# Kernel tuning notes

Hardware: AMD Instinct MI355X
Metric: run time of the kernel (lower is better)

## Reference

```python
import jax, jax.numpy as jnp
import numpy as np

B, K = 16, 50
IN_CH, N_CLASSES, N_ANCH = 256, 80, 3
STRIDE, FSIZE, IGNORE_THRE = 8, 76, 0.7
N_CH = 5 + N_CLASSES
ANCHORS = np.array([[10,13],[16,30],[33,23],[30,61],[62,45],[59,119],[116,90],[156,198],[373,326]], np.float32)
ALL_GRID = ANCHORS / STRIDE            # all 9 anchors in grid units
ANCH_MASK = np.array([0, 1, 2])        # layer_no = 2
MASKED = ALL_GRID[ANCH_MASK]           # (3,2) anchors used by this head


def setup_inputs():
    key = jax.random.key(0)
    k1, k2, k3, k4, k5, k6 = jax.random.split(key, 6)
    xin = jax.random.normal(k1, (B, IN_CH, FSIZE, FSIZE), jnp.float32)
    cls = jax.random.randint(k2, (B, K), 0, N_CLASSES).astype(jnp.float32)
    xy = jax.random.uniform(k3, (B, K, 2), minval=0.05, maxval=0.95)
    wh = jax.random.uniform(k4, (B, K, 2), minval=0.02, maxval=0.30)
    labels = jnp.concatenate([cls[..., None], xy, wh], -1)   # (B,K,5) [cls,xc,yc,w,h]
    oc = N_ANCH * N_CH
    conv_w = jax.random.normal(k5, (oc, IN_CH), jnp.float32) * 0.01
    conv_b = jax.random.normal(k6, (oc,), jnp.float32) * 0.01
    return {"xin": xin, "labels": labels, "conv_w": conv_w, "conv_b": conv_b}


def _yolo(xin, conv_w, conv_b, labels):
    f, C = FSIZE, N_CLASSES
    # 1x1 conv == channel matmul
    raw = jnp.einsum('bchw,oc->bohw', xin, conv_w) + conv_b[None, :, None, None]
    raw = raw.reshape(B, N_ANCH, N_CH, f, f).transpose(0, 1, 3, 4, 2)  # (B,A,f,f,85)
    # sigmoid on x,y,obj,cls; w,h stay raw
    out = jnp.concatenate([jax.nn.sigmoid(raw[..., :2]), raw[..., 2:4], jax.nn.sigmoid(raw[..., 4:])], -1)

    grid = jnp.arange(f, dtype=jnp.float32)
    mw = jnp.asarray(MASKED[:, 0]); mh = jnp.asarray(MASKED[:, 1])
    px = out[..., 0] + grid[None, None, None, :]
    py = out[..., 1] + grid[None, None, :, None]
    pw = jnp.exp(out[..., 2]) * mw[None, :, None, None]
    ph = jnp.exp(out[..., 3]) * mh[None, :, None, None]
    pred = jax.lax.stop_gradient(jnp.stack([px, py, pw, ph], -1))  # detached, like torch .data

    labels = jax.lax.stop_gradient(labels)
    valid = labels.sum(-1) > 0                  # (B,K) padding rows are all-zero
    tx = labels[..., 1] * f; ty = labels[..., 2] * f
    tw = labels[..., 3] * f; th = labels[..., 4] * f
    ii = tx.astype(jnp.int32); jj = ty.astype(jnp.int32)

    # anchor matching: IoU of [0,0,w,h] truth vs [0,0,aw,ah] ref anchors (corners at origin)
    aw = jnp.asarray(ALL_GRID[:, 0]); ah = jnp.asarray(ALL_GRID[:, 1])
    inter_a = jnp.minimum(tw[..., None], aw) * jnp.minimum(th[..., None], ah)  # (B,K,9)
    iou_a = inter_a / (tw[..., None] * th[..., None] + aw * ah - inter_a)
    best_n_all = jnp.argmax(iou_a, -1)
    best_n = best_n_all % 3
    best_mask = (best_n_all == ANCH_MASK[0]) | (best_n_all == ANCH_MASK[1]) | (best_n_all == ANCH_MASK[2])

    # pred-vs-truth IoU in cxcywh form (xyxy=False)
    pa = pred.reshape(B, -1, 4)                 # (B, A*f*f, 4)
    tb = jnp.stack([tx, ty, tw, th], -1)        # (B, K, 4)
    tl = jnp.maximum(pa[:, :, None, :2] - pa[:, :, None, 2:] * 0.5, tb[:, None, :, :2] - tb[:, None, :, 2:] * 0.5)
    br = jnp.minimum(pa[:, :, None, :2] + pa[:, :, None, 2:] * 0.5, tb[:, None, :, :2] + tb[:, None, :, 2:] * 0.5)
    en = jnp.all(tl < br, -1)
    inter = jnp.prod(br - tl, -1) * en
    area_p = pa[..., 2] * pa[..., 3]; area_t = tb[..., 2] * tb[..., 3]
    iou_p = inter / (area_p[:, :, None] + area_t[:, None, :] - inter)
    iou_p = jnp.where(valid[:, None, :], iou_p, 0.0)
    ignore = (iou_p.max(-1) > IGNORE_THRE).reshape(B, N_ANCH, f, f)
    obj_mask = 1.0 - ignore.astype(jnp.float32)

    # scatter positive targets; non-selected rows routed out-of-bounds and dropped
    sel = valid & best_mask
    bb = jnp.where(sel, jnp.arange(B)[:, None], B)
    obj_mask = obj_mask.at[bb, best_n, jj, ii].set(1.0, mode='drop')
    tgt_mask = jnp.zeros((B, N_ANCH, f, f, 4 + C)).at[bb, best_n, jj, ii].set(1.0, mode='drop')
    scale = jnp.sqrt(2.0 - tw * th / (f * f))
    tgt_scale = jnp.zeros((B, N_ANCH, f, f, 2)).at[bb, best_n, jj, ii].set(
        jnp.broadcast_to(scale[..., None], (B, K, 2)), mode='drop')
    tvals = jnp.concatenate([
        (tx - ii)[..., None], (ty - jj)[..., None],
        jnp.log(tw / mw[best_n] + 1e-16)[..., None],
        jnp.log(th / mh[best_n] + 1e-16)[..., None],
        jnp.ones((B, K, 1), jnp.float32),
        jax.nn.one_hot(labels[..., 0].astype(jnp.int32), C)], -1)  # (B,K,85)
    target = jnp.zeros((B, N_ANCH, f, f, N_CH)).at[bb, best_n, jj, ii].set(tvals, mode='drop')

    oxy = out[..., :2] * tgt_mask[..., :2]
    owh = out[..., 2:4] * tgt_mask[..., 2:4] * tgt_scale
    oob = out[..., 4] * obj_mask
    ocl = out[..., 5:] * tgt_mask[..., 4:]
    txy = target[..., :2] * tgt_mask[..., :2]
    twh = target[..., 2:4] * tgt_mask[..., 2:4] * tgt_scale
    tob = target[..., 4] * obj_mask
    tcl = target[..., 5:] * tgt_mask[..., 4:]

    def bce(p, t, w=None):
        pc = jnp.clip(p, 1e-12, 1.0 - 1e-7)
        e = -(t * jnp.log(pc) + (1.0 - t) * jnp.log(1.0 - pc))
        if w is not None:
            e = e * w
        return e.sum()

    loss_xy = bce(oxy, txy, tgt_scale * tgt_scale)
    loss_wh = 0.5 * jnp.sum((owh - twh) ** 2)
    loss_obj = bce(oob, tob)
    loss_cls = bce(ocl, tcl)
    out_m = jnp.concatenate([oxy, owh, oob[..., None], ocl], -1)
    tgt_m = jnp.concatenate([txy, twh, tob[..., None], tcl], -1)
    loss_l2 = jnp.sum((out_m - tgt_m) ** 2)
    loss = loss_xy + loss_wh + loss_obj + loss_cls
    return loss, loss_xy, loss_wh, loss_obj, loss_cls, loss_l2, out_m


def reference(xin, labels, conv_w, conv_b):
    return _yolo(xin, conv_w, conv_b, labels)
```

## Files before the change

### kernel.cpp

```cpp
#include <hip/hip_runtime.h>
#include <hip/hip_bf16.h>

#define B_   16
#define K_   50
#define CIN  256
#define F_   76
#define A_   3
#define NCH  85
#define OC   255
#define HW   (F_*F_)
#define NBLK (B_*F_)
#define NCELL (A_*F_)
#define SLAB (F_*NCH)

#define WS_BIAS_F 32768
#define WS_LAB_F  33024
#define WS_PART_F 45824
#define WS_W15_F  55552

typedef __attribute__((ext_vector_type(8))) short short8;
typedef __attribute__((ext_vector_type(4))) float f32x4;

__device__ __constant__ float AW9[9] = {1.25f, 2.0f, 4.125f, 3.75f, 7.75f, 7.375f, 14.5f, 19.5f, 46.625f};
__device__ __constant__ float AH9[9] = {1.625f, 3.75f, 2.875f, 7.625f, 5.625f, 14.875f, 11.25f, 24.75f, 40.75f};

__device__ __forceinline__ unsigned short f2bf(float f) {
    union { float f; unsigned int u; } v; v.f = f;
    unsigned int r = v.u + 0x7fffu + ((v.u >> 16) & 1u);
    return (unsigned short)(r >> 16);
}
__device__ __forceinline__ float bf2f(unsigned short b) {
    union { unsigned int u; float f; } v; v.u = ((unsigned int)b) << 16;
    return v.f;
}
__device__ __forceinline__ float sigm(float r) { return 1.0f / (1.0f + __expf(-r)); }
__device__ __forceinline__ float bce_t(float p, float tv) {
    float pc = fminf(fmaxf(p, 1e-12f), 1.0f - 1e-7f);
    return -(tv * __logf(pc) + (1.0f - tv) * __logf(1.0f - pc));
}

__global__ void prep_kernel(const float* __restrict__ conv_w, const float* __restrict__ conv_b,
                            const float* __restrict__ labels, float* __restrict__ ws) {
    int bid = blockIdx.x, t = threadIdx.x;
    if (bid < 256) {
        float v = (t < OC) ? conv_w[t * CIN + bid] : 0.0f;
        ((unsigned short*)ws)[bid * 256 + t] = f2bf(v);
    } else if (bid == 256) {
        ws[WS_BIAS_F + t] = (t < OC) ? conv_b[t] : 0.0f;
    } else if (bid == 257) {
        for (int idx = t; idx < B_ * K_; idx += 256) {
            const float* L = labels + idx * 5;
            float cls = L[0], xc = L[1], yc = L[2], wl = L[3], hl = L[4];
            float ssum = cls + xc + yc + wl + hl;
            float validf = (ssum > 0.0f) ? 1.0f : 0.0f;
            float tx = xc * F_, ty = yc * F_, tw = wl * F_, th = hl * F_;
            int ii = (int)tx, jj = (int)ty;
            float tarea = tw * th;
            float best = -1.0f; int bn = 0;
            #pragma unroll
            for (int n = 0; n < 9; n++) {
                float inter = fminf(tw, AW9[n]) * fminf(th, AH9[n]);
                float iou = inter / (tarea + AW9[n] * AH9[n] - inter);
                if (iou > best) { best = iou; bn = n; }
            }
            int a = bn % 3;
            bool self = (validf != 0.0f) && (bn < 3);
            float* R = ws + WS_LAB_F + idx * 16;
            R[0] = tx; R[1] = ty; R[2] = tw; R[3] = th;
            R[4] = validf; R[5] = self ? (float)a : -1.0f; R[6] = (float)ii; R[7] = (float)jj;
            R[8] = tx - (float)ii; R[9] = ty - (float)jj;
            R[10] = __logf(tw / AW9[a] + 1e-16f);
            R[11] = __logf(th / AH9[a] + 1e-16f);
            R[12] = sqrtf(2.0f - tarea / (float)HW);
            R[13] = cls; R[14] = 0.0f; R[15] = 0.0f;
        }
    } else {
        unsigned short* wf = (unsigned short*)(ws + WS_W15_F);
        for (int idx = t; idx < 4096; idx += 256) {
            int ks = idx >> 9, lane = (idx >> 3) & 63, jj = idx & 7;
            int row = lane & 15;
            int k = ks * 32 + (lane >> 4) * 8 + jj;
            float v = 0.0f;
            if (row < 15) v = conv_w[((row / 5) * NCH + (row % 5)) * CIN + k];
            wf[idx] = f2bf(v);
        }
    }
}

__global__ __launch_bounds__(320) void fused_kernel(const float* __restrict__ xin,
                                                    const float* __restrict__ ws,
                                                    float* __restrict__ d_out,
                                                    float* __restrict__ part) {
    __shared__ float raw5S[15 * F_];
    __shared__ float4 LAB[K_ * 4];
    __shared__ int   flagS[NCELL];
    __shared__ float omvS[NCELL];
    __shared__ float xcolS[256];
    __shared__ float redS[5][5];

    const int t = threadIdx.x;
    const int w = t >> 6, lane = t & 63;
    const int b = blockIdx.x / F_;
    const int j = blockIdx.x % F_;
    const int lr = lane & 15, q = lane >> 4;
    const int col0 = (w < 4) ? (w << 4) : 60;

    if (t < K_ * 4) LAB[t] = ((const float4*)(ws + WS_LAB_F + b * (K_ * 16)))[t];

    const unsigned short* wf15 = (const unsigned short*)(ws + WS_W15_F);
    short8 afr[8];
    #pragma unroll
    for (int ks = 0; ks < 8; ks++)
        afr[ks] = *(const short8*)&wf15[(ks * 64 + lane) * 8];

    f32x4 acc = (f32x4){0.0f, 0.0f, 0.0f, 0.0f};
    const float* xbase = xin + (size_t)b * CIN * HW + j * F_ + col0 + lr;
    #pragma unroll
    for (int ks = 0; ks < 8; ks++) {
        int kb = ks * 32 + q * 8;
        float xv[8];
        #pragma unroll
        for (int jj = 0; jj < 8; jj++) xv[jj] = xbase[(size_t)(kb + jj) * HW];
        union { short8 s; __hip_bfloat162 h[4]; } u;
        #pragma unroll
        for (int p = 0; p < 4; p++)
            u.h[p] = __float22bfloat162_rn(make_float2(xv[2 * p], xv[2 * p + 1]));
        acc = __builtin_amdgcn_mfma_f32_16x16x32_bf16(afr[ks], u.s, acc, 0, 0, 0);
    }

    const float* biasg = ws + WS_BIAS_F;
    if (w < 4 || lr >= 4) {
        #pragma unroll
        for (int r = 0; r < 4; r++) {
            int row = q * 4 + r;
            if (row < 15) {
                int o = (row / 5) * NCH + (row % 5);
                raw5S[row * F_ + col0 + lr] = acc[r] + biasg[o];
            }
        }
    }
    __syncthreads();

    float lxy = 0.0f, lwh = 0.0f, lobj = 0.0f, lcls = 0.0f, l2 = 0.0f;
    if (t < NCELL) {
        int a = t / F_, i = t - a * F_;
        float x   = sigm(raw5S[(a * 5 + 0) * F_ + i]);
        float y   = sigm(raw5S[(a * 5 + 1) * F_ + i]);
        float wr  = raw5S[(a * 5 + 2) * F_ + i];
        float hr  = raw5S[(a * 5 + 3) * F_ + i];
        float obj = sigm(raw5S[(a * 5 + 4) * F_ + i]);

        float px = x + (float)i, py = y + (float)j;
        float pw = __expf(wr) * AW9[a], ph = __expf(hr) * AH9[a];
        float hpw = pw * 0.5f, hph = ph * 0.5f;
        float areap = pw * ph;
        float fa_t = (float)a, fi_t = (float)i, fj_t = (float)j;

        float maxiou = 0.0f; int mk = -1;
        #pragma unroll 2
        for (int k = 0; k < K_; k++) {
            float4 A0 = LAB[4 * k + 0];
            float4 A1 = LAB[4 * k + 1];
            float tx = A0.x, ty = A0.y, tw = A0.z, th = A0.w;
            float tlx = fmaxf(px - hpw, tx - tw * 0.5f);
            float tly = fmaxf(py - hph, ty - th * 0.5f);
            float brx = fminf(px + hpw, tx + tw * 0.5f);
            float bry = fminf(py + hph, ty + th * 0.5f);
            float iw = brx - tlx, ih = bry - tly;
            float inter = (iw > 0.0f && ih > 0.0f) ? iw * ih : 0.0f;
            float iou = __fdividef(inter, areap + tw * th - inter);
            iou = (A1.x != 0.0f) ? iou : 0.0f;
            maxiou = fmaxf(maxiou, iou);
            bool match = (A1.y == fa_t) & (A1.z == fi_t) & (A1.w == fj_t);
            mk = match ? k : mk;
        }
        float objmask = (maxiou > 0.7f) ? 0.0f : 1.0f;

        if (mk >= 0) {
            float4 B0 = LAB[4 * mk + 2];
            float4 B1 = LAB[4 * mk + 3];
            float sc = B1.x, sc2 = sc * sc;
            float txv = B0.x, tyv = B0.y, twv = B0.z, thv = B0.w;
            lxy = (bce_t(x, txv) + bce_t(y, tyv)) * sc2;
            float dw = wr - twv, dh = hr - thv;
            lwh = 0.5f * sc2 * (dw * dw + dh * dh);
            float pco = fminf(fmaxf(obj, 1e-12f), 1.0f - 1e-7f);
            lobj = -__logf(pco);
            float dx = x - txv, dy = y - tyv, dob = obj - 1.0f;
            l2 = dx * dx + dy * dy + sc2 * (dw * dw + dh * dh) + dob * dob;
            flagS[t] = mk + 1;
            omvS[t]  = obj;
        } else {
            float oo = obj * objmask;
            if (objmask != 0.0f) {
                float pco = fminf(obj, 1.0f - 1e-7f);
                lobj = -__logf(1.0f - pco);
            }
            l2 = oo * oo;
            flagS[t] = 0;
            omvS[t]  = oo;
        }
    }
    __syncthreads();

    for (int a = 0; a < A_; a++) {
        float2* dst = (float2*)(d_out + 6 + (size_t)((b * A_ + a) * F_ + j) * SLAB);
        for (int idx2 = t; idx2 < SLAB / 2; idx2 += 320) {
            int p = idx2 << 1;
            int i0 = p / NCH, c0 = p - i0 * NCH;
            int i1 = i0, c1 = c0 + 1;
            if (c1 == NCH) { i1++; c1 = 0; }
            float v0 = (c0 == 4) ? omvS[a * F_ + i0] : 0.0f;
            float v1 = (c1 == 4) ? omvS[a * F_ + i1] : 0.0f;
            dst[idx2] = make_float2(v0, v1);
        }
    }
    __threadfence_block();
    __syncthreads();

    const unsigned short* Wtg = (const unsigned short*)ws;
    for (int k = 0; k < K_; k++) {
        float4 A1 = LAB[4 * k + 1];
        int fa = (int)A1.y;
        if (fa < 0) continue;
        if ((int)A1.w != j) continue;
        int fi = (int)A1.z;
        int cell = fa * F_ + fi;
        if (flagS[cell] != k + 1) continue;

        if (t < 256) xcolS[t] = xin[((size_t)b * CIN + t) * HW + j * F_ + fi];
        __syncthreads();
        float4 B1 = LAB[4 * k + 3];
        float sc = B1.x; int cl = (int)B1.y;
        if (t < NCH) {
            float v; int chout;
            if (t < 80) {
                int o = fa * NCH + 5 + t;
                float accv = biasg[o];
                #pragma unroll 8
                for (int kk = 0; kk < 256; kk++)
                    accv += bf2f(Wtg[kk * 256 + o]) * xcolS[kk];
                float p = sigm(accv);
                float tcv = (t == cl) ? 1.0f : 0.0f;
                lcls += bce_t(p, tcv);
                float d = p - tcv;
                l2 += d * d;
                v = p; chout = 5 + t;
            } else {
                int ch = t - 80;
                float raw = raw5S[(fa * 5 + ch) * F_ + fi];
                v = (ch == 2 || ch == 3) ? raw * sc : sigm(raw);
                chout = ch;
            }
            d_out[6 + (size_t)((b * A_ + fa) * F_ + j) * SLAB + fi * NCH + chout] = v;
        }
        __syncthreads();
    }

    #pragma unroll
    for (int off = 32; off > 0; off >>= 1) {
        lxy  += __shfl_down(lxy, off);
        lwh  += __shfl_down(lwh, off);
        lobj += __shfl_down(lobj, off);
        lcls += __shfl_down(lcls, off);
        l2   += __shfl_down(l2, off);
    }
    if (lane == 0) {
        redS[w][0] = lxy; redS[w][1] = lwh; redS[w][2] = lobj;
        redS[w][3] = lcls; redS[w][4] = l2;
    }
    __syncthreads();
    if (t == 0) {
        float* P = part + (size_t)blockIdx.x * 8;
        #pragma unroll
        for (int q2 = 0; q2 < 5; q2++)
            P[q2] = redS[0][q2] + redS[1][q2] + redS[2][q2] + redS[3][q2] + redS[4][q2];
    }
}

__global__ void finish_kernel(const float* __restrict__ part, float* __restrict__ d_out) {
    int t = threadIdx.x;
    float s0 = 0, s1 = 0, s2 = 0, s3 = 0, s4 = 0;
    for (int bidx = t; bidx < NBLK; bidx += 256) {
        const float* P = part + (size_t)bidx * 8;
        s0 += P[0]; s1 += P[1]; s2 += P[2]; s3 += P[3]; s4 += P[4];
    }
    #pragma unroll
    for (int off = 32; off > 0; off >>= 1) {
        s0 += __shfl_down(s0, off); s1 += __shfl_down(s1, off);
        s2 += __shfl_down(s2, off); s3 += __shfl_down(s3, off);
        s4 += __shfl_down(s4, off);
    }
    __shared__ float red[4][5];
    if ((t & 63) == 0) {
        int w = t >> 6;
        red[w][0] = s0; red[w][1] = s1; red[w][2] = s2; red[w][3] = s3; red[w][4] = s4;
    }
    __syncthreads();
    if (t == 0) {
        float r0 = red[0][0] + red[1][0] + red[2][0] + red[3][0];
        float r1 = red[0][1] + red[1][1] + red[2][1] + red[3][1];
        float r2 = red[0][2] + red[1][2] + red[2][2] + red[3][2];
        float r3 = red[0][3] + red[1][3] + red[2][3] + red[3][3];
        float r4 = red[0][4] + red[1][4] + red[2][4] + red[3][4];
        d_out[0] = r0 + r1 + r2 + r3;
        d_out[1] = r0; d_out[2] = r1; d_out[3] = r2; d_out[4] = r3; d_out[5] = r4;
    }
}

extern "C" void kernel_launch(void* const* d_in, const int* in_sizes, int n_in,
                              void* d_out, int out_size, void* d_ws, size_t ws_size,
                              hipStream_t stream) {
    const float* xin    = (const float*)d_in[0];
    const float* labels = (const float*)d_in[1];
    const float* conv_w = (const float*)d_in[2];
    const float* conv_b = (const float*)d_in[3];
    float* out  = (float*)d_out;
    float* ws   = (float*)d_ws;
    float* part = ws + WS_PART_F;

    prep_kernel<<<259, 256, 0, stream>>>(conv_w, conv_b, labels, ws);
    fused_kernel<<<NBLK, 320, 0, stream>>>(xin, ws, out, part);
    finish_kernel<<<1, 256, 0, stream>>>(part, out);
}
```

Baseline: 212.4 us.

## Split fused kernel into FP32 conv-loss, slab writer, and sparse target kernels

Replaces the per-row fused kernel, which ran a bf16 MFMA for 15 box channels and then wrote a slab and handled targets, with a pipeline of four kernels. The first does an FP32 CUDA-core 15-channel conv over 128-pixel tiles with two channel halves, evaluates IoU and losses for all three anchors per pixel, and appends matched targets to a list through an atomic counter. A separate writer kernel emits the mostly-zero output slabs with float4 stores, and a sparse kernel recomputes the 80 class logits for each matched cell in FP32 straight from conv_w. This removes the full bf16 weight transpose and spreads the output writes and target work across more blocks, at the cost of an extra global round trip for objectness values and more kernel launches. Results may differ slightly from before because the math is now FP32 instead of bf16.

```diff
diff --git a/kernel.cpp b/kernel.cpp
--- a/kernel.cpp
+++ b/kernel.cpp
@@ -9,30 +9,26 @@
 #define NCH  85
 #define OC   255
 #define HW   (F_*F_)
-#define NBLK (B_*F_)
-#define NCELL (A_*F_)
 #define SLAB (F_*NCH)
 
-#define WS_BIAS_F 32768
-#define WS_LAB_F  33024
-#define WS_PART_F 45824
-#define WS_W15_F  55552
-
-typedef __attribute__((ext_vector_type(8))) short short8;
-typedef __attribute__((ext_vector_type(4))) float f32x4;
+#define WS_BIAS_F 0
+#define WS_LAB_F  256
+#define WS_W15P_F 13056
+#define WS_B15_F  17152
+#define WS_CNT_F  17168
+#define WS_REC_F  17184
+#define WS_PART_F 23584
+#define WS_OMV_F  35872
+#define WS_END_F  313120
+
+#define NTL   46
+#define NCONV (B_*NTL)
+#define NREC  800
+#define NROW  (NCONV + NREC)
 
 __device__ __constant__ float AW9[9] = {1.25f, 2.0f, 4.125f, 3.75f, 7.75f, 7.375f, 14.5f, 19.5f, 46.625f};
 __device__ __constant__ float AH9[9] = {1.625f, 3.75f, 2.875f, 7.625f, 5.625f, 14.875f, 11.25f, 24.75f, 40.75f};
 
-__device__ __forceinline__ unsigned short f2bf(float f) {
-    union { float f; unsigned int u; } v; v.f = f;
-    unsigned int r = v.u + 0x7fffu + ((v.u >> 16) & 1u);
-    return (unsigned short)(r >> 16);
-}
-__device__ __forceinline__ float bf2f(unsigned short b) {
-    union { unsigned int u; float f; } v; v.u = ((unsigned int)b) << 16;
-    return v.f;
-}
 __device__ __forceinline__ float sigm(float r) { return 1.0f / (1.0f + __expf(-r)); }
 __device__ __forceinline__ float bce_t(float p, float tv) {
     float pc = fminf(fmaxf(p, 1e-12f), 1.0f - 1e-7f);
@@ -42,12 +38,9 @@
 __global__ void prep_kernel(const float* __restrict__ conv_w, const float* __restrict__ conv_b,
                             const float* __restrict__ labels, float* __restrict__ ws) {
     int bid = blockIdx.x, t = threadIdx.x;
-    if (bid < 256) {
-        float v = (t < OC) ? conv_w[t * CIN + bid] : 0.0f;
-        ((unsigned short*)ws)[bid * 256 + t] = f2bf(v);
-    } else if (bid == 256) {
+    if (bid == 0) {
         ws[WS_BIAS_F + t] = (t < OC) ? conv_b[t] : 0.0f;
-    } else if (bid == 257) {
+    } else if (bid == 1) {
         for (int idx = t; idx < B_ * K_; idx += 256) {
             const float* L = labels + idx * 5;
             float cls = L[0], xc = L[1], yc = L[2], wl = L[3], hl = L[4];
@@ -75,213 +68,235 @@
             R[13] = cls; R[14] = 0.0f; R[15] = 0.0f;
         }
     } else {
-        unsigned short* wf = (unsigned short*)(ws + WS_W15_F);
         for (int idx = t; idx < 4096; idx += 256) {
-            int ks = idx >> 9, lane = (idx >> 3) & 63, jj = idx & 7;
-            int row = lane & 15;
-            int k = ks * 32 + (lane >> 4) * 8 + jj;
+            int c = idx >> 4, r = idx & 15;
             float v = 0.0f;
-            if (row < 15) v = conv_w[((row / 5) * NCH + (row % 5)) * CIN + k];
-            wf[idx] = f2bf(v);
-        }
-    }
-}
-
-__global__ __launch_bounds__(320) void fused_kernel(const float* __restrict__ xin,
-                                                    const float* __restrict__ ws,
-                                                    float* __restrict__ d_out,
-                                                    float* __restrict__ part) {
-    __shared__ float raw5S[15 * F_];
+            if (r < 15) v = conv_w[((r / 5) * NCH + (r % 5)) * CIN + c];
+            ws[WS_W15P_F + idx] = v;
+        }
+        if (t < 16) ws[WS_B15_F + t] = (t < 15) ? conv_b[(t / 5) * NCH + (t % 5)] : 0.0f;
+        if (t == 16) *(int*)(ws + WS_CNT_F) = 0;
+    }
+}
+
+__global__ __launch_bounds__(256) void convloss_kernel(const float* __restrict__ xin,
+                                                       float* __restrict__ ws) {
     __shared__ float4 LAB[K_ * 4];
-    __shared__ int   flagS[NCELL];
-    __shared__ float omvS[NCELL];
-    __shared__ float xcolS[256];
-    __shared__ float redS[5][5];
+    __shared__ float accS[128][16];
+    __shared__ float redS[2][4];
 
     const int t = threadIdx.x;
-    const int w = t >> 6, lane = t & 63;
-    const int b = blockIdx.x / F_;
-    const int j = blockIdx.x % F_;
-    const int lr = lane & 15, q = lane >> 4;
-    const int col0 = (w < 4) ? (w << 4) : 60;
+    const int blk = blockIdx.x;
+    const int b = blk / NTL, tile = blk - b * NTL;
+    const int ph = t & 127;
+    const int p0 = tile * 128 + ph;
+    const bool ok = p0 < HW;
+    const int p = ok ? p0 : HW - 1;
+    const int half = __builtin_amdgcn_readfirstlane(t) >> 7;
 
     if (t < K_ * 4) LAB[t] = ((const float4*)(ws + WS_LAB_F + b * (K_ * 16)))[t];
 
-    const unsigned short* wf15 = (const unsigned short*)(ws + WS_W15_F);
-    short8 afr[8];
-    #pragma unroll
-    for (int ks = 0; ks < 8; ks++)
-        afr[ks] = *(const short8*)&wf15[(ks * 64 + lane) * 8];
-
-    f32x4 acc = (f32x4){0.0f, 0.0f, 0.0f, 0.0f};
-    const float* xbase = xin + (size_t)b * CIN * HW + j * F_ + col0 + lr;
-    #pragma unroll
-    for (int ks = 0; ks < 8; ks++) {
-        int kb = ks * 32 + q * 8;
-        float xv[8];
-        #pragma unroll
-        for (int jj = 0; jj < 8; jj++) xv[jj] = xbase[(size_t)(kb + jj) * HW];
-        union { short8 s; __hip_bfloat162 h[4]; } u;
-        #pragma unroll
-        for (int p = 0; p < 4; p++)
-            u.h[p] = __float22bfloat162_rn(make_float2(xv[2 * p], xv[2 * p + 1]));
-        acc = __builtin_amdgcn_mfma_f32_16x16x32_bf16(afr[ks], u.s, acc, 0, 0, 0);
-    }
-
-    const float* biasg = ws + WS_BIAS_F;
-    if (w < 4 || lr >= 4) {
-        #pragma unroll
-        for (int r = 0; r < 4; r++) {
-            int row = q * 4 + r;
-            if (row < 15) {
-                int o = (row / 5) * NCH + (row % 5);
-                raw5S[row * F_ + col0 + lr] = acc[r] + biasg[o];
-            }
-        }
-    }
-    __syncthreads();
-
-    float lxy = 0.0f, lwh = 0.0f, lobj = 0.0f, lcls = 0.0f, l2 = 0.0f;
-    if (t < NCELL) {
-        int a = t / F_, i = t - a * F_;
-        float x   = sigm(raw5S[(a * 5 + 0) * F_ + i]);
-        float y   = sigm(raw5S[(a * 5 + 1) * F_ + i]);
-        float wr  = raw5S[(a * 5 + 2) * F_ + i];
-        float hr  = raw5S[(a * 5 + 3) * F_ + i];
-        float obj = sigm(raw5S[(a * 5 + 4) * F_ + i]);
-
-        float px = x + (float)i, py = y + (float)j;
-        float pw = __expf(wr) * AW9[a], ph = __expf(hr) * AH9[a];
-        float hpw = pw * 0.5f, hph = ph * 0.5f;
-        float areap = pw * ph;
-        float fa_t = (float)a, fi_t = (float)i, fj_t = (float)j;
-
-        float maxiou = 0.0f; int mk = -1;
+    const float* xp = xin + (size_t)b * CIN * HW + (size_t)half * 128 * HW + p;
+    const float* Wp = ws + WS_W15P_F + half * 128 * 16;
+
+    float acc[15];
+    #pragma unroll
+    for (int r = 0; r < 15; r++) acc[r] = 0.0f;
+
+    float xv[8];
+    #pragma unroll
+    for (int u = 0; u < 8; u++) xv[u] = xp[(size_t)u * HW];
+    #pragma unroll 1
+    for (int c8 = 0; c8 < 16; c8++) {
+        float xn[8];
+        const int cnx = (c8 < 15) ? (c8 + 1) : 15;
+        #pragma unroll
+        for (int u = 0; u < 8; u++) xn[u] = xp[(size_t)(cnx * 8 + u) * HW];
+        #pragma unroll
+        for (int u = 0; u < 8; u++) {
+            const float xvu = xv[u];
+            const float* wrow = Wp + (c8 * 8 + u) * 16;
+            #pragma unroll
+            for (int r = 0; r < 15; r++) acc[r] = fmaf(xvu, wrow[r], acc[r]);
+        }
+        #pragma unroll
+        for (int u = 0; u < 8; u++) xv[u] = xn[u];
+    }
+
+    if (half) {
+        #pragma unroll
+        for (int r = 0; r < 15; r++) accS[ph][r] = acc[r];
+    }
+    __syncthreads();
+
+    float lxy = 0.0f, lwh = 0.0f, lobj = 0.0f, l2 = 0.0f;
+    if (t < 128 && ok) {
+        #pragma unroll
+        for (int r = 0; r < 15; r++) acc[r] += accS[ph][r] + ws[WS_B15_F + r];
+        const int j = p / F_, i = p - j * F_;
+        const float fi_t = (float)i, fj_t = (float)j;
+        float X[3], Y[3], WR[3], HR[3], OB[3], HPW[3], HPH[3], ARP[3], PX[3], PY[3];
+        #pragma unroll
+        for (int a = 0; a < 3; a++) {
+            X[a] = sigm(acc[a * 5 + 0]); Y[a] = sigm(acc[a * 5 + 1]);
+            WR[a] = acc[a * 5 + 2]; HR[a] = acc[a * 5 + 3]; OB[a] = sigm(acc[a * 5 + 4]);
+            PX[a] = X[a] + fi_t; PY[a] = Y[a] + fj_t;
+            float pw = __expf(WR[a]) * AW9[a], phh = __expf(HR[a]) * AH9[a];
+            HPW[a] = pw * 0.5f; HPH[a] = phh * 0.5f; ARP[a] = pw * phh;
+        }
+        float mxi[3] = {0.0f, 0.0f, 0.0f}; int mk[3] = {-1, -1, -1};
         #pragma unroll 2
         for (int k = 0; k < K_; k++) {
-            float4 A0 = LAB[4 * k + 0];
-            float4 A1 = LAB[4 * k + 1];
+            float4 A0 = LAB[4 * k], A1 = LAB[4 * k + 1];
             float tx = A0.x, ty = A0.y, tw = A0.z, th = A0.w;
-            float tlx = fmaxf(px - hpw, tx - tw * 0.5f);
-            float tly = fmaxf(py - hph, ty - th * 0.5f);
-            float brx = fminf(px + hpw, tx + tw * 0.5f);
-            float bry = fminf(py + hph, ty + th * 0.5f);
-            float iw = brx - tlx, ih = bry - tly;
-            float inter = (iw > 0.0f && ih > 0.0f) ? iw * ih : 0.0f;
-            float iou = __fdividef(inter, areap + tw * th - inter);
-            iou = (A1.x != 0.0f) ? iou : 0.0f;
-            maxiou = fmaxf(maxiou, iou);
-            bool match = (A1.y == fa_t) & (A1.z == fi_t) & (A1.w == fj_t);
-            mk = match ? k : mk;
-        }
-        float objmask = (maxiou > 0.7f) ? 0.0f : 1.0f;
-
-        if (mk >= 0) {
-            float4 B0 = LAB[4 * mk + 2];
-            float4 B1 = LAB[4 * mk + 3];
-            float sc = B1.x, sc2 = sc * sc;
-            float txv = B0.x, tyv = B0.y, twv = B0.z, thv = B0.w;
-            lxy = (bce_t(x, txv) + bce_t(y, tyv)) * sc2;
-            float dw = wr - twv, dh = hr - thv;
-            lwh = 0.5f * sc2 * (dw * dw + dh * dh);
-            float pco = fminf(fmaxf(obj, 1e-12f), 1.0f - 1e-7f);
-            lobj = -__logf(pco);
-            float dx = x - txv, dy = y - tyv, dob = obj - 1.0f;
-            l2 = dx * dx + dy * dy + sc2 * (dw * dw + dh * dh) + dob * dob;
-            flagS[t] = mk + 1;
-            omvS[t]  = obj;
-        } else {
-            float oo = obj * objmask;
-            if (objmask != 0.0f) {
-                float pco = fminf(obj, 1.0f - 1e-7f);
-                lobj = -__logf(1.0f - pco);
+            float tlx0 = tx - tw * 0.5f, tly0 = ty - th * 0.5f;
+            float brx0 = tx + tw * 0.5f, bry0 = ty + th * 0.5f;
+            float ta = tw * th, va = A1.x;
+            #pragma unroll
+            for (int a = 0; a < 3; a++) {
+                float tlx = fmaxf(PX[a] - HPW[a], tlx0);
+                float tly = fmaxf(PY[a] - HPH[a], tly0);
+                float brx = fminf(PX[a] + HPW[a], brx0);
+                float bry = fminf(PY[a] + HPH[a], bry0);
+                float iw = brx - tlx, ih = bry - tly;
+                float inter = (iw > 0.0f && ih > 0.0f) ? iw * ih : 0.0f;
+                float iou = __fdividef(inter, ARP[a] + ta - inter);
+                iou = (va != 0.0f) ? iou : 0.0f;
+                mxi[a] = fmaxf(mxi[a], iou);
+                bool match = (A1.y == (float)a) & (A1.z == fi_t) & (A1.w == fj_t);
+                mk[a] = match ? k : mk[a];
             }
-            l2 = oo * oo;
-            flagS[t] = 0;
-            omvS[t]  = oo;
-        }
-    }
-    __syncthreads();
-
-    for (int a = 0; a < A_; a++) {
-        float2* dst = (float2*)(d_out + 6 + (size_t)((b * A_ + a) * F_ + j) * SLAB);
-        for (int idx2 = t; idx2 < SLAB / 2; idx2 += 320) {
-            int p = idx2 << 1;
-            int i0 = p / NCH, c0 = p - i0 * NCH;
-            int i1 = i0, c1 = c0 + 1;
-            if (c1 == NCH) { i1++; c1 = 0; }
-            float v0 = (c0 == 4) ? omvS[a * F_ + i0] : 0.0f;
-            float v1 = (c1 == 4) ? omvS[a * F_ + i1] : 0.0f;
-            dst[idx2] = make_float2(v0, v1);
-        }
-    }
-    __threadfence_block();
-    __syncthreads();
-
-    const unsigned short* Wtg = (const unsigned short*)ws;
-    for (int k = 0; k < K_; k++) {
-        float4 A1 = LAB[4 * k + 1];
-        int fa = (int)A1.y;
-        if (fa < 0) continue;
-        if ((int)A1.w != j) continue;
-        int fi = (int)A1.z;
-        int cell = fa * F_ + fi;
-        if (flagS[cell] != k + 1) continue;
-
-        if (t < 256) xcolS[t] = xin[((size_t)b * CIN + t) * HW + j * F_ + fi];
-        __syncthreads();
-        float4 B1 = LAB[4 * k + 3];
-        float sc = B1.x; int cl = (int)B1.y;
-        if (t < NCH) {
-            float v; int chout;
-            if (t < 80) {
-                int o = fa * NCH + 5 + t;
-                float accv = biasg[o];
-                #pragma unroll 8
-                for (int kk = 0; kk < 256; kk++)
-                    accv += bf2f(Wtg[kk * 256 + o]) * xcolS[kk];
-                float p = sigm(accv);
-                float tcv = (t == cl) ? 1.0f : 0.0f;
-                lcls += bce_t(p, tcv);
-                float d = p - tcv;
-                l2 += d * d;
-                v = p; chout = 5 + t;
+        }
+        #pragma unroll
+        for (int a = 0; a < 3; a++) {
+            float objmask = (mxi[a] > 0.7f) ? 0.0f : 1.0f;
+            float omv;
+            if (mk[a] >= 0) {
+                float4 B0 = LAB[4 * mk[a] + 2];
+                float4 B1 = LAB[4 * mk[a] + 3];
+                float sc = B1.x, sc2 = sc * sc;
+                lxy += (bce_t(X[a], B0.x) + bce_t(Y[a], B0.y)) * sc2;
+                float dw = WR[a] - B0.z, dh = HR[a] - B0.w;
+                lwh += 0.5f * sc2 * (dw * dw + dh * dh);
+                float pco = fminf(fmaxf(OB[a], 1e-12f), 1.0f - 1e-7f);
+                lobj += -__logf(pco);
+                float dx = X[a] - B0.x, dy = Y[a] - B0.y, dob = OB[a] - 1.0f;
+                l2 += dx * dx + dy * dy + sc2 * (dw * dw + dh * dh) + dob * dob;
+                omv = OB[a];
+                int ridx = atomicAdd((int*)(ws + WS_CNT_F), 1);
+                float* R = ws + WS_REC_F + ridx * 8;
+                R[0] = (float)b; R[1] = (float)a; R[2] = (float)p; R[3] = (float)mk[a];
+                R[4] = X[a]; R[5] = Y[a]; R[6] = WR[a] * sc; R[7] = HR[a] * sc;
             } else {
-                int ch = t - 80;
-                float raw = raw5S[(fa * 5 + ch) * F_ + fi];
-                v = (ch == 2 || ch == 3) ? raw * sc : sigm(raw);
-                chout = ch;
+                float oo = OB[a] * objmask;
+                if (objmask != 0.0f) {
+                    float pco = fminf(OB[a], 1.0f - 1e-7f);
+                    lobj += -__logf(1.0f - pco);
+                }
+                l2 += oo * oo;
+                omv = oo;
             }
-            d_out[6 + (size_t)((b * A_ + fa) * F_ + j) * SLAB + fi * NCH + chout] = v;
-        }
-        __syncthreads();
+            ws[WS_OMV_F + (size_t)(b * A_ + a) * HW + p] = omv;
+        }
     }
 
     #pragma unroll
     for (int off = 32; off > 0; off >>= 1) {
-        lxy  += __shfl_down(lxy, off);
-        lwh  += __shfl_down(lwh, off);
-        lobj += __shfl_down(lobj, off);
-        lcls += __shfl_down(lcls, off);
-        l2   += __shfl_down(l2, off);
-    }
-    if (lane == 0) {
-        redS[w][0] = lxy; redS[w][1] = lwh; redS[w][2] = lobj;
-        redS[w][3] = lcls; redS[w][4] = l2;
+        lxy += __shfl_down(lxy, off); lwh += __shfl_down(lwh, off);
+        lobj += __shfl_down(lobj, off); l2 += __shfl_down(l2, off);
+    }
+    if (t < 128 && (t & 63) == 0) {
+        redS[t >> 6][0] = lxy; redS[t >> 6][1] = lwh;
+        redS[t >> 6][2] = lobj; redS[t >> 6][3] = l2;
     }
     __syncthreads();
     if (t == 0) {
-        float* P = part + (size_t)blockIdx.x * 8;
-        #pragma unroll
-        for (int q2 = 0; q2 < 5; q2++)
-            P[q2] = redS[0][q2] + redS[1][q2] + redS[2][q2] + redS[3][q2] + redS[4][q2];
-    }
-}
-
-__global__ void finish_kernel(const float* __restrict__ part, float* __restrict__ d_out) {
+        float* P = ws + WS_PART_F + (size_t)blk * 8;
+        P[0] = redS[0][0] + redS[1][0];
+        P[1] = redS[0][1] + redS[1][1];
+        P[2] = redS[0][2] + redS[1][2];
+        P[3] = 0.0f;
+        P[4] = redS[0][3] + redS[1][3];
+    }
+}
+
+__global__ __launch_bounds__(256) void writer_kernel(const float* __restrict__ ws,
+                                                     float* __restrict__ d_out) {
+    const int t = threadIdx.x;
+    const int s = blockIdx.x;
+    const int baj = s / F_, j = s - baj * F_;
+    const float* om = ws + WS_OMV_F + (size_t)baj * HW + j * F_;
+    float* slab = d_out + 6 + (size_t)s * SLAB;
+    if (t == 0) { slab[0] = 0.0f; slab[1] = 0.0f; slab[6458] = 0.0f; slab[6459] = 0.0f; }
+    float4* dst4 = (float4*)(slab + 2);
+    for (int n = t; n < 1614; n += 256) {
+        int f0 = 2 + 4 * n;
+        int p = f0 / 85, r = f0 - 85 * p;
+        float4 v = make_float4(0.0f, 0.0f, 0.0f, 0.0f);
+        if (r >= 1 && r <= 4) ((float*)&v)[4 - r] = om[p];
+        dst4[n] = v;
+    }
+}
+
+__global__ __launch_bounds__(256) void sparse_kernel(const float* __restrict__ xin,
+                                                     const float* __restrict__ conv_w,
+                                                     float* __restrict__ ws,
+                                                     float* __restrict__ d_out) {
+    __shared__ float xcolS[256];
+    __shared__ float rr[4][2];
+    const int t = threadIdx.x;
+    const int idx = blockIdx.x;
+    float* P = ws + WS_PART_F + (size_t)(NCONV + idx) * 8;
+    const int cnt = *(const int*)(ws + WS_CNT_F);
+    if (idx >= cnt) { if (t < 8) P[t] = 0.0f; return; }
+    const float* R = ws + WS_REC_F + idx * 8;
+    const int b = (int)R[0], a = (int)R[1], p = (int)R[2], k = (int)R[3];
+    const int j = p / F_, i = p - j * F_;
+    xcolS[t] = xin[((size_t)b * CIN + t) * HW + p];
+    __syncthreads();
+    const float* Lr = ws + WS_LAB_F + (b * K_ + k) * 16;
+    const int cl = (int)Lr[13];
+    float* cell = d_out + 6 + (size_t)((b * A_ + a) * F_ + j) * SLAB + i * NCH;
+    float lcls = 0.0f, l2 = 0.0f;
+    if (t < 80) {
+        const int o = a * NCH + 5 + t;
+        const float4* wr4 = (const float4*)(conv_w + (size_t)o * CIN);
+        float a0 = 0, a1 = 0, a2 = 0, a3 = 0;
+        #pragma unroll 8
+        for (int q = 0; q < 64; q++) {
+            float4 wv = wr4[q];
+            a0 = fmaf(wv.x, xcolS[q * 4 + 0], a0);
+            a1 = fmaf(wv.y, xcolS[q * 4 + 1], a1);
+            a2 = fmaf(wv.z, xcolS[q * 4 + 2], a2);
+            a3 = fmaf(wv.w, xcolS[q * 4 + 3], a3);
+        }
+        float accv = ws[WS_BIAS_F + o] + ((a0 + a1) + (a2 + a3));
+        float pc = sigm(accv);
+        float tcv = (t == cl) ? 1.0f : 0.0f;
+        lcls = bce_t(pc, tcv);
+        float d = pc - tcv; l2 = d * d;
+        cell[5 + t] = pc;
+    } else if (t < 84) {
+        cell[t - 80] = R[4 + (t - 80)];
+    }
+    #pragma unroll
+    for (int off = 32; off > 0; off >>= 1) {
+        lcls += __shfl_down(lcls, off); l2 += __shfl_down(l2, off);
+    }
+    if ((t & 63) == 0) { rr[t >> 6][0] = lcls; rr[t >> 6][1] = l2; }
+    __syncthreads();
+    if (t == 0) {
+        P[0] = 0.0f; P[1] = 0.0f; P[2] = 0.0f;
+        P[3] = rr[0][0] + rr[1][0] + rr[2][0] + rr[3][0];
+        P[4] = rr[0][1] + rr[1][1] + rr[2][1] + rr[3][1];
+    }
+}
+
+__global__ void finish_kernel(const float* __restrict__ ws, float* __restrict__ d_out) {
     int t = threadIdx.x;
+    const float* part = ws + WS_PART_F;
     float s0 = 0, s1 = 0, s2 = 0, s3 = 0, s4 = 0;
-    for (int bidx = t; bidx < NBLK; bidx += 256) {
+    for (int bidx = t; bidx < NROW; bidx += 256) {
         const float* P = part + (size_t)bidx * 8;
         s0 += P[0]; s1 += P[1]; s2 += P[2]; s3 += P[3]; s4 += P[4];
     }
@@ -315,11 +330,12 @@
     const float* labels = (const float*)d_in[1];
     const float* conv_w = (const float*)d_in[2];
     const float* conv_b = (const float*)d_in[3];
-    float* out  = (float*)d_out;
-    float* ws   = (float*)d_ws;
-    float* part = ws + WS_PART_F;
-
-    prep_kernel<<<259, 256, 0, stream>>>(conv_w, conv_b, labels, ws);
-    fused_kernel<<<NBLK, 320, 0, stream>>>(xin, ws, out, part);
-    finish_kernel<<<1, 256, 0, stream>>>(part, out);
-}
+    float* out = (float*)d_out;
+    float* ws  = (float*)d_ws;
+
+    prep_kernel<<<3, 256, 0, stream>>>(conv_w, conv_b, labels, ws);
+    convloss_kernel<<<NCONV, 256, 0, stream>>>(xin, ws);
+    writer_kernel<<<B_ * A_ * F_, 256, 0, stream>>>(ws, out);
+    sparse_kernel<<<NREC, 256, 0, stream>>>(xin, conv_w, ws, out);
+    finish_kernel<<<1, 256, 0, stream>>>(ws, out);
+}
```

Result: slower. 224.7 us (+5.8%).
